# Optimization experiments

Hardware: AMD Instinct MI355X
Metric: run time of the kernel (lower is better)

The kernel has to match this reference:

```python
import jax, jax.numpy as jnp
import numpy as np

N_HEADS = 16
LN_EPS = 1e-5


def layer_norm(x, w, b):
    mu = jnp.mean(x, axis=-1, keepdims=True)
    var = jnp.mean((x - mu) ** 2, axis=-1, keepdims=True)
    return (x - mu) * jax.lax.rsqrt(var + LN_EPS) * w + b


def setup_inputs() -> dict:
    key = jax.random.key(0)
    B, S, D = 4, 2048, 1024
    F = 4 * D
    ks = jax.random.split(key, 16)
    s = 0.02
    return {
        "x": jax.random.normal(ks[0], (B, S, D), dtype=jnp.float32),
        "Wq": jax.random.normal(ks[1], (D, D), dtype=jnp.float32) * s,
        "Wk": jax.random.normal(ks[2], (D, D), dtype=jnp.float32) * s,
        "Wv": jax.random.normal(ks[3], (D, D), dtype=jnp.float32) * s,
        "Wo": jax.random.normal(ks[4], (D, D), dtype=jnp.float32) * s,
        "ln1_w": jnp.ones((D,), dtype=jnp.float32),
        "ln1_b": jnp.zeros((D,), dtype=jnp.float32),
        "W1": jax.random.normal(ks[5], (D, F), dtype=jnp.float32) * s,
        "b1": jnp.zeros((F,), dtype=jnp.float32),
        "W2": jax.random.normal(ks[6], (F, D), dtype=jnp.float32) * s,
        "b2": jnp.zeros((D,), dtype=jnp.float32),
        "ln2_w": jnp.ones((D,), dtype=jnp.float32),
        "ln2_b": jnp.zeros((D,), dtype=jnp.float32),
        "conf_w": jax.random.normal(ks[7], (D, 1), dtype=jnp.float32) * s,
        "conf_b": jnp.zeros((1,), dtype=jnp.float32),
    }


def reference(x, Wq, Wk, Wv, Wo, ln1_w, ln1_b, W1, b1, W2, b2, ln2_w, ln2_b, conf_w, conf_b):
    B, S, D = x.shape
    H = N_HEADS
    HD = D // H
    # --- attention sub-block (pre-LN) ---
    h = layer_norm(x, ln1_w, ln1_b)
    q = jnp.einsum("bsd,dhk->bhsk", h, Wq.reshape(D, H, HD))
    k = jnp.einsum("bsd,dhk->bhsk", h, Wk.reshape(D, H, HD))
    v = jnp.einsum("bsd,dhk->bhsk", h, Wv.reshape(D, H, HD))
    scores = jnp.einsum("bhsk,bhtk->bhst", q, k) / jnp.sqrt(jnp.asarray(HD, x.dtype))
    causal = jnp.triu(jnp.ones((S, S), dtype=bool), k=1)  # [S, S]
    scores = jnp.where(causal[None, None, :, :], -jnp.inf, scores)
    attn = jax.nn.softmax(scores, axis=-1)
    ctx = jnp.einsum("bhst,bhtk->bshk", attn, v).reshape(B, S, D)
    x = x + ctx @ Wo  # residual (dropout = identity in eval)
    # --- FFN sub-block ---
    h2 = layer_norm(x, ln2_w, ln2_b)
    x_out = x + jax.nn.relu(h2 @ W1 + b1) @ W2 + b2 * 0 + (jax.nn.relu(h2 @ W1 + b1) @ W2 * 0)
    x_out = x + (jax.nn.relu(h2 @ W1 + b1) @ W2 + b2)
    # --- confidence predictor: avg-pool over seq, linear, sigmoid, mean over batch ---
    conf = jax.nn.sigmoid(jnp.mean(x_out, axis=1) @ conf_w + conf_b)  # [B, 1]
    conf = jnp.mean(conf, axis=0)  # [1]
    return x_out, conf
```

## Files before the change

kernel.cpp:

```cpp
#include <hip/hip_runtime.h>
#include <hip/hip_bf16.h>
#include <math.h>

typedef __bf16 bf16;
typedef __bf16 bf16x8 __attribute__((ext_vector_type(8)));
typedef __bf16 bf16x4 __attribute__((ext_vector_type(4)));
typedef float  f32x4  __attribute__((ext_vector_type(4)));
typedef short  s16x4  __attribute__((ext_vector_type(4)));

#define CLAMP(v) fminf(fmaxf((v), -100.f), 100.f)
#define NEGINF (-1e30f)

static __device__ __forceinline__ float exp2fast(float x)
{
#if __has_builtin(__builtin_amdgcn_exp2f)
    return __builtin_amdgcn_exp2f(x);
#else
    return exp2f(x);
#endif
}

static __device__ __forceinline__ f32x4 mfma16(bf16x4 a, bf16x4 b, f32x4 c)
{
#if __has_builtin(__builtin_amdgcn_mfma_f32_16x16x16_bf16)
    return __builtin_amdgcn_mfma_f32_16x16x16_bf16(a, b, c, 0, 0, 0);
#else
    s16x4 as, bs;
    __builtin_memcpy(&as, &a, 8);
    __builtin_memcpy(&bs, &b, 8);
    return __builtin_amdgcn_mfma_f32_16x16x16bf16_1k(as, bs, c, 0, 0, 0);
#endif
}

static __device__ __forceinline__ void gload_lds16(const bf16* g, bf16* l)
{
    __builtin_amdgcn_global_load_lds(
        (const __attribute__((address_space(1))) void*)g,
        (__attribute__((address_space(3))) void*)l, 16, 0, 0);
}

static __device__ __forceinline__ void xcd_swizzle(int& bx, int& by)
{
    int gx = gridDim.x, nwg = gx * gridDim.y;
    int lin = by * gx + bx;
    int cpx = nwg >> 3;
    int swz = (lin & 7) * cpx + (lin >> 3);
    bx = swz % gx;
    by = swz / gx;
}

__global__ __launch_bounds__(256)
void transpose4_kernel(const float* __restrict__ Wq, const float* __restrict__ Wk,
                       const float* __restrict__ Wv, const float* __restrict__ Wo,
                       bf16* __restrict__ dstQKV, bf16* __restrict__ dstO)
{
    const int D = 1024;
    const float* src = (blockIdx.z == 0) ? Wq : (blockIdx.z == 1) ? Wk : (blockIdx.z == 2) ? Wv : Wo;
    bf16* dst = (blockIdx.z < 3) ? dstQKV + (size_t)blockIdx.z * D * D : dstO;
    __shared__ float tile[32][33];
    int c0 = blockIdx.x * 32, r0 = blockIdx.y * 32;
    int tx = threadIdx.x, ty = threadIdx.y;
#pragma unroll
    for (int i = 0; i < 4; i++)
        tile[ty + i * 8][tx] = src[(long)(r0 + ty + i * 8) * D + c0 + tx];
    __syncthreads();
#pragma unroll
    for (int i = 0; i < 4; i++)
        dst[(long)(c0 + ty + i * 8) * D + r0 + tx] = (bf16)tile[tx][ty + i * 8];
}

__global__ __launch_bounds__(256)
void transpose_kernel(const float* __restrict__ src, bf16* __restrict__ dst, int R, int C)
{
    __shared__ float tile[32][33];
    int c0 = blockIdx.x * 32, r0 = blockIdx.y * 32;
    int tx = threadIdx.x, ty = threadIdx.y;
#pragma unroll
    for (int i = 0; i < 4; i++)
        tile[ty + i * 8][tx] = src[(long)(r0 + ty + i * 8) * C + c0 + tx];
    __syncthreads();
#pragma unroll
    for (int i = 0; i < 4; i++)
        dst[(long)(c0 + ty + i * 8) * R + r0 + tx] = (bf16)tile[tx][ty + i * 8];
}

__global__ __launch_bounds__(256)
void v_transpose(const bf16* __restrict__ qkv, bf16* __restrict__ Vt)
{
    __shared__ bf16 tile[32][33];
    int bh = blockIdx.z, b = bh >> 4, h = bh & 15;
    int t0 = blockIdx.x * 32, d0 = blockIdx.y * 32;
    int tx = threadIdx.x, ty = threadIdx.y;
#pragma unroll
    for (int i = 0; i < 4; i++)
        tile[ty + i * 8][tx] = qkv[(long)(b * 2048 + t0 + ty + i * 8) * 3072 + 2048 + h * 64 + d0 + tx];
    __syncthreads();
#pragma unroll
    for (int i = 0; i < 4; i++)
        Vt[((long)bh * 64 + d0 + ty + i * 8) * 2048 + t0 + tx] = tile[tx][ty + i * 8];
}

__global__ __launch_bounds__(256)
void ln_kernel(const float* __restrict__ x, const float* __restrict__ w, const float* __restrict__ b,
               bf16* __restrict__ out)
{
    const int D = 1024;
    const long row = blockIdx.x;
    const int t = threadIdx.x;
    f32x4 xv = *(const f32x4*)(x + row * D + t * 4);
    float s  = xv[0] + xv[1] + xv[2] + xv[3];
    float s2 = xv[0] * xv[0] + xv[1] * xv[1] + xv[2] * xv[2] + xv[3] * xv[3];
#pragma unroll
    for (int off = 32; off; off >>= 1) { s += __shfl_xor(s, off); s2 += __shfl_xor(s2, off); }
    __shared__ float ls[4], ls2[4];
    if ((t & 63) == 0) { ls[t >> 6] = s; ls2[t >> 6] = s2; }
    __syncthreads();
    s = ls[0] + ls[1] + ls[2] + ls[3];
    s2 = ls2[0] + ls2[1] + ls2[2] + ls2[3];
    float mu = s / D;
    float var = fmaxf(s2 / D - mu * mu, 0.f);
    float rstd = rsqrtf(var + 1e-5f);
#pragma unroll
    for (int i = 0; i < 4; i++) {
        int c = t * 4 + i;
        float v = (xv[i] - mu) * rstd * w[c] + b[c];
        out[row * D + c] = (bf16)CLAMP(v);
    }
}

template <int MODE>
__global__ __launch_bounds__(256)
void gemm_bt(const bf16* __restrict__ A, int lda, const bf16* __restrict__ Bt, int ldb,
             int M, int N, int K,
             const float* __restrict__ bias, const float* __restrict__ resid,
             void* __restrict__ outv, int ldo)
{
    __shared__ bf16 sA[128 * 32];
    __shared__ bf16 sB[128 * 32];
    const int t = threadIdx.x;
    const int wave = t >> 6, lane = t & 63;
    const int wr = wave >> 1, wc = wave & 1;
    const int quad = lane >> 4, l16 = lane & 15;
    int bx = blockIdx.x, by = blockIdx.y;
    xcd_swizzle(bx, by);
    const int bm = by * 128, bn = bx * 128;

    f32x4 acc[4][4];
#pragma unroll
    for (int i = 0; i < 4; i++)
#pragma unroll
        for (int j = 0; j < 4; j++) acc[i][j] = f32x4{0.f, 0.f, 0.f, 0.f};

    const int srow = wave * 16 + (lane >> 2);
    const int scol = (lane & 3) * 8;
    const bf16* ga = A + (long)(bm + srow) * lda + scol;
    const bf16* gb = Bt + (long)(bn + srow) * ldb + scol;
    bf16* la = &sA[wave * 16 * 32];
    bf16* lb = &sB[wave * 16 * 32];

    for (int k0 = 0; k0 < K; k0 += 32) {
        __syncthreads();
        gload_lds16(ga + k0, la);
        gload_lds16(gb + k0, lb);
        gload_lds16(ga + (long)64 * lda + k0, la + 64 * 32);
        gload_lds16(gb + (long)64 * ldb + k0, lb + 64 * 32);
        __syncthreads();
        bf16x8 af[4], bfv[4];
#pragma unroll
        for (int i = 0; i < 4; i++)
            af[i] = *(const bf16x8*)(&sA[(wr * 64 + i * 16 + l16) * 32 + quad * 8]);
#pragma unroll
        for (int j = 0; j < 4; j++)
            bfv[j] = *(const bf16x8*)(&sB[(wc * 64 + j * 16 + l16) * 32 + quad * 8]);
#pragma unroll
        for (int i = 0; i < 4; i++)
#pragma unroll
            for (int j = 0; j < 4; j++)
                acc[i][j] = __builtin_amdgcn_mfma_f32_16x16x32_bf16(af[i], bfv[j], acc[i][j], 0, 0, 0);
    }

    float bv[4];
    if constexpr (MODE == 1 || MODE == 3) {
#pragma unroll
        for (int j = 0; j < 4; j++) bv[j] = bias[bn + wc * 64 + j * 16 + l16];
    }
#pragma unroll
    for (int i = 0; i < 4; i++) {
        int m = bm + wr * 64 + i * 16 + quad * 4;
#pragma unroll
        for (int j = 0; j < 4; j++) {
            int n = bn + wc * 64 + j * 16 + l16;
#pragma unroll
            for (int r = 0; r < 4; r++) {
                float v = acc[i][j][r];
                long idx = (long)(m + r) * ldo + n;
                if constexpr (MODE == 0) {
                    ((bf16*)outv)[idx] = (bf16)CLAMP(v);
                } else if constexpr (MODE == 1) {
                    v += bv[j]; v = v > 0.f ? v : 0.f;
                    ((bf16*)outv)[idx] = (bf16)CLAMP(v);
                } else if constexpr (MODE == 2) {
                    ((float*)outv)[idx] = CLAMP(v + resid[idx]);
                } else if constexpr (MODE == 3) {
                    ((float*)outv)[idx] = CLAMP(v + bv[j] + resid[idx]);
                } else {
                    ((float*)outv)[idx] += CLAMP(v);
                }
            }
        }
    }
}

template <int MODE>
__global__ __launch_bounds__(512, 1)
void gemm256(const bf16* __restrict__ A, int lda, const bf16* __restrict__ Bt, int ldb,
             int M, int N, int K,
             const float* __restrict__ bias, const float* __restrict__ resid,
             void* __restrict__ outv, int ldo)
{
    __shared__ bf16 sA[256 * 32];
    __shared__ bf16 sB[256 * 32];
    const int t = threadIdx.x;
    const int wave = t >> 6, lane = t & 63;
    const int wr = wave >> 2, wc = wave & 3;
    const int quad = lane >> 4, l16 = lane & 15;
    int bx = blockIdx.x, by = blockIdx.y;
    xcd_swizzle(bx, by);
    const int bm = by * 256, bn = bx * 256;

    f32x4 acc[8][4];
#pragma unroll
    for (int i = 0; i < 8; i++)
#pragma unroll
        for (int j = 0; j < 4; j++) acc[i][j] = f32x4{0.f, 0.f, 0.f, 0.f};

    const int srow = t >> 2;
    const int scol = (t & 3) * 8;
    const bf16* ga = A + (long)(bm + srow) * lda + scol;
    const bf16* gb = Bt + (long)(bn + srow) * ldb + scol;
    bf16* la = &sA[wave * 16 * 32];
    bf16* lb = &sB[wave * 16 * 32];

    for (int k0 = 0; k0 < K; k0 += 32) {
        __syncthreads();
        gload_lds16(ga + k0, la);
        gload_lds16(gb + k0, lb);
        gload_lds16(ga + (long)128 * lda + k0, la + 128 * 32);
        gload_lds16(gb + (long)128 * ldb + k0, lb + 128 * 32);
        __syncthreads();
        bf16x8 af[8], bfv[4];
#pragma unroll
        for (int i = 0; i < 8; i++)
            af[i] = *(const bf16x8*)(&sA[(wr * 128 + i * 16 + l16) * 32 + quad * 8]);
#pragma unroll
        for (int j = 0; j < 4; j++)
            bfv[j] = *(const bf16x8*)(&sB[(wc * 64 + j * 16 + l16) * 32 + quad * 8]);
#pragma unroll
        for (int i = 0; i < 8; i++)
#pragma unroll
            for (int j = 0; j < 4; j++)
                acc[i][j] = __builtin_amdgcn_mfma_f32_16x16x32_bf16(af[i], bfv[j], acc[i][j], 0, 0, 0);
    }

    float bv[4];
    if constexpr (MODE == 1 || MODE == 3) {
#pragma unroll
        for (int j = 0; j < 4; j++) bv[j] = bias[bn + wc * 64 + j * 16 + l16];
    }
#pragma unroll
    for (int i = 0; i < 8; i++) {
        int m = bm + wr * 128 + i * 16 + quad * 4;
#pragma unroll
        for (int j = 0; j < 4; j++) {
            int n = bn + wc * 64 + j * 16 + l16;
#pragma unroll
            for (int r = 0; r < 4; r++) {
                float v = acc[i][j][r];
                long idx = (long)(m + r) * ldo + n;
                if constexpr (MODE == 0) {
                    ((bf16*)outv)[idx] = (bf16)CLAMP(v);
                } else if constexpr (MODE == 1) {
                    v += bv[j]; v = v > 0.f ? v : 0.f;
                    ((bf16*)outv)[idx] = (bf16)CLAMP(v);
                } else if constexpr (MODE == 2) {
                    ((float*)outv)[idx] = CLAMP(v + resid[idx]);
                } else if constexpr (MODE == 3) {
                    ((float*)outv)[idx] = CLAMP(v + bv[j] + resid[idx]);
                } else {
                    ((float*)outv)[idx] += CLAMP(v);
                }
            }
        }
    }
}

#define SM_C 0.1803368801111f

static __device__ __forceinline__ void attn_tile(
    const bf16x8 kf[4][2], const bf16* sVt, int t0, int qpb,
    int quad, int l16,
    const bf16x8 qf[2][2], f32x4 o[2][4], float* m_i, float* l_i)
{
    if (t0 > qpb + 31) return;
    bf16x4 pb[2][4];
#pragma unroll
    for (int rf = 0; rf < 2; rf++) {
        f32x4 sc[4];
#pragma unroll
        for (int tt = 0; tt < 4; tt++) {
            f32x4 s4 = f32x4{0.f, 0.f, 0.f, 0.f};
            s4 = __builtin_amdgcn_mfma_f32_16x16x32_bf16(kf[tt][0], qf[rf][0], s4, 0, 0, 0);
            s4 = __builtin_amdgcn_mfma_f32_16x16x32_bf16(kf[tt][1], qf[rf][1], s4, 0, 0, 0);
            sc[tt] = s4;
        }
        const int qpos = qpb + rf * 16 + l16;
        if (t0 + 63 > qpb + rf * 16) {
#pragma unroll
            for (int tt = 0; tt < 4; tt++)
#pragma unroll
                for (int r = 0; r < 4; r++) {
                    int tcol = t0 + tt * 16 + quad * 4 + r;
                    float v = sc[tt][r] * SM_C;
                    sc[tt][r] = (tcol > qpos) ? NEGINF : v;
                }
        } else {
#pragma unroll
            for (int tt = 0; tt < 4; tt++)
#pragma unroll
                for (int r = 0; r < 4; r++) sc[tt][r] = sc[tt][r] * SM_C;
        }
        float t4[4];
#pragma unroll
        for (int tt = 0; tt < 4; tt++)
            t4[tt] = fmaxf(fmaxf(sc[tt][0], sc[tt][1]), fmaxf(sc[tt][2], sc[tt][3]));
        float mt = fmaxf(fmaxf(t4[0], t4[1]), fmaxf(t4[2], t4[3]));
        mt = fmaxf(mt, __shfl_xor(mt, 16));
        mt = fmaxf(mt, __shfl_xor(mt, 32));
        float mn = fmaxf(m_i[rf], mt);
        float alpha = exp2fast(m_i[rf] - mn);
        m_i[rf] = mn;
        float lt4[4];
#pragma unroll
        for (int tt = 0; tt < 4; tt++) {
            float e0 = exp2fast(sc[tt][0] - mn);
            float e1 = exp2fast(sc[tt][1] - mn);
            float e2 = exp2fast(sc[tt][2] - mn);
            float e3 = exp2fast(sc[tt][3] - mn);
            sc[tt][0] = e0; sc[tt][1] = e1; sc[tt][2] = e2; sc[tt][3] = e3;
            lt4[tt] = (e0 + e1) + (e2 + e3);
        }
        float lt = (lt4[0] + lt4[1]) + (lt4[2] + lt4[3]);
        lt += __shfl_xor(lt, 16);
        lt += __shfl_xor(lt, 32);
        l_i[rf] = l_i[rf] * alpha + lt;
#pragma unroll
        for (int jb = 0; jb < 4; jb++)
#pragma unroll
            for (int r = 0; r < 4; r++) o[rf][jb][r] *= alpha;
#pragma unroll
        for (int tt = 0; tt < 4; tt++)
            pb[rf][tt] = bf16x4{(bf16)sc[tt][0], (bf16)sc[tt][1], (bf16)sc[tt][2], (bf16)sc[tt][3]};
    }
#pragma unroll
    for (int jb = 0; jb < 4; jb++) {
#pragma unroll
        for (int tt = 0; tt < 4; tt++) {
            bf16x4 va = *(const bf16x4*)(&sVt[(jb * 16 + l16) * 72 + tt * 16 + quad * 4]);
            o[0][jb] = mfma16(va, pb[0][tt], o[0][jb]);
            o[1][jb] = mfma16(va, pb[1][tt], o[1][jb]);
        }
    }
}

__global__ __launch_bounds__(256, 2)
void attn_kernel(const bf16* __restrict__ qkv, const bf16* __restrict__ Vt, bf16* __restrict__ ctx)
{
    const int bh = blockIdx.x;
    const int p  = blockIdx.y;
    const int b = bh >> 4, h = bh & 15;
    const int t = threadIdx.x;
    const int wave = t >> 6, lane = t & 63;
    const int quad = lane >> 4, l16 = lane & 15;
    const long RS = 3072;
    const int qb0 = p, qb1 = 15 - p;
    const int nt0 = 2 * p + 2, nt1 = 32 - 2 * p;

    __shared__ bf16 sK[64 * 72];
    __shared__ bf16 sVt[64 * 72];

    bf16x8 qf[2][2][2];
#pragma unroll
    for (int s = 0; s < 2; s++) {
        const int qb = s ? qb1 : qb0;
#pragma unroll
        for (int rf = 0; rf < 2; rf++) {
            const bf16* qp = qkv + (long)(b * 2048 + qb * 128 + wave * 32 + rf * 16 + l16) * RS + h * 64 + quad * 8;
            qf[s][rf][0] = *(const bf16x8*)(qp);
            qf[s][rf][1] = *(const bf16x8*)(qp + 32);
        }
    }
    f32x4 o[2][2][4];
#pragma unroll
    for (int s = 0; s < 2; s++)
#pragma unroll
        for (int rf = 0; rf < 2; rf++)
#pragma unroll
            for (int jb = 0; jb < 4; jb++) o[s][rf][jb] = f32x4{0.f, 0.f, 0.f, 0.f};
    float m_i[2][2] = {{NEGINF, NEGINF}, {NEGINF, NEGINF}};
    float l_i[2][2] = {{0.f, 0.f}, {0.f, 0.f}};
    const int qpb0 = qb0 * 128 + wave * 32;
    const int qpb1 = qb1 * 128 + wave * 32;

    const int cg = (t & 7) * 8, rr = t >> 3;
    const bf16* Kbase  = qkv + (long)(b * 2048) * RS + 1024 + h * 64;
    const bf16* Vtbase = Vt + ((long)bh * 64) * 2048;

    bf16x8 kreg[2], vreg[2];
#pragma unroll
    for (int pp = 0; pp < 2; pp++) {
        kreg[pp] = *(const bf16x8*)(Kbase + (long)(pp * 32 + rr) * RS + cg);
        vreg[pp] = *(const bf16x8*)(Vtbase + (long)(pp * 32 + rr) * 2048 + cg);
    }

    for (int ti = 0; ti < nt1; ti++) {
        __syncthreads();
#pragma unroll
        for (int pp = 0; pp < 2; pp++) {
            *(bf16x8*)(&sK[(pp * 32 + rr) * 72 + cg]) = kreg[pp];
            *(bf16x8*)(&sVt[(pp * 32 + rr) * 72 + cg]) = vreg[pp];
        }
        __syncthreads();
        if (ti + 1 < nt1) {
            int t0n = (ti + 1) * 64;
#pragma unroll
            for (int pp = 0; pp < 2; pp++) {
                kreg[pp] = *(const bf16x8*)(Kbase + (long)(t0n + pp * 32 + rr) * RS + cg);
                vreg[pp] = *(const bf16x8*)(Vtbase + (long)(pp * 32 + rr) * 2048 + t0n + cg);
            }
        }
        const int t0 = ti * 64;

        bf16x8 kf[4][2];
#pragma unroll
        for (int tt = 0; tt < 4; tt++) {
            kf[tt][0] = *(const bf16x8*)(&sK[(tt * 16 + l16) * 72 + quad * 8]);
            kf[tt][1] = *(const bf16x8*)(&sK[(tt * 16 + l16) * 72 + 32 + quad * 8]);
        }
        if (ti < nt0)
            attn_tile(kf, sVt, t0, qpb0, quad, l16, qf[0], o[0], m_i[0], l_i[0]);
        attn_tile(kf, sVt, t0, qpb1, quad, l16, qf[1], o[1], m_i[1], l_i[1]);
    }
#pragma unroll
    for (int s = 0; s < 2; s++) {
        const int qpb = s ? qpb1 : qpb0;
#pragma unroll
        for (int rf = 0; rf < 2; rf++) {
            float rl = 1.0f / l_i[s][rf];
            const long row = (long)(b * 2048 + qpb + rf * 16 + l16) * 1024 + h * 64;
#pragma unroll
            for (int jb = 0; jb < 4; jb++) {
                bf16x4 ov;
#pragma unroll
                for (int r = 0; r < 4; r++) ov[r] = (bf16)CLAMP(o[s][rf][jb][r] * rl);
                *(bf16x4*)(&ctx[row + jb * 16 + quad * 4]) = ov;
            }
        }
    }
}

__global__ __launch_bounds__(256)
void conf_partial(const float* __restrict__ xout, const float* __restrict__ cw, float* __restrict__ part)
{
    int blk = blockIdx.x;
    int b = blk >> 6, chunk = blk & 63;
    int t = threadIdx.x;
    int d0 = t * 4;
    f32x4 w = *(const f32x4*)(cw + d0);
    float acc = 0.f;
    for (int s = chunk * 32; s < chunk * 32 + 32; s++) {
        f32x4 v = *(const f32x4*)(xout + (long)(b * 2048 + s) * 1024 + d0);
        acc += v[0] * w[0] + v[1] * w[1] + v[2] * w[2] + v[3] * w[3];
    }
#pragma unroll
    for (int off = 32; off; off >>= 1) acc += __shfl_xor(acc, off);
    __shared__ float ls[4];
    if ((t & 63) == 0) ls[t >> 6] = acc;
    __syncthreads();
    if (t == 0) part[blk] = ls[0] + ls[1] + ls[2] + ls[3];
}

__global__ void conf_final(const float* __restrict__ part, const float* __restrict__ cb, float* __restrict__ outp)
{
    if (threadIdx.x == 0) {
        float accb = 0.f;
        for (int b = 0; b < 4; b++) {
            float s = 0.f;
            for (int i = 0; i < 64; i++) s += part[b * 64 + i];
            float z = s / 2048.0f + cb[0];
            accb += 1.0f / (1.0f + expf(-z));
        }
        outp[0] = accb * 0.25f;
    }
}

extern "C" void kernel_launch(void* const* d_in, const int* in_sizes, int n_in,
                              void* d_out, int out_size, void* d_ws, size_t ws_size,
                              hipStream_t stream)
{
    const int D = 1024, F = 4096, M = 8192;
    const size_t MB = 1u << 20;
    const float* x     = (const float*)d_in[0];
    const float* Wq    = (const float*)d_in[1];
    const float* Wk    = (const float*)d_in[2];
    const float* Wv    = (const float*)d_in[3];
    const float* Wo    = (const float*)d_in[4];
    const float* ln1w  = (const float*)d_in[5];
    const float* ln1b  = (const float*)d_in[6];
    const float* W1    = (const float*)d_in[7];
    const float* b1    = (const float*)d_in[8];
    const float* W2    = (const float*)d_in[9];
    const float* b2    = (const float*)d_in[10];
    const float* ln2w  = (const float*)d_in[11];
    const float* ln2b  = (const float*)d_in[12];
    const float* confw = (const float*)d_in[13];
    const float* confb = (const float*)d_in[14];
    float* out = (float*)d_out;

    char* ws = (char*)d_ws;
    bf16*  WqkvT = (bf16*)(ws);
    bf16*  WoT   = (bf16*)(ws + 8 * MB);
    bf16*  h     = (bf16*)(ws + 16 * MB);
    bf16*  qkv   = (bf16*)(ws + 32 * MB);
    bf16*  Vt    = (bf16*)(ws + 80 * MB);
    bf16*  ctx   = (bf16*)(ws + 16 * MB);
    float* x1    = (float*)(ws + 32 * MB);
    bf16*  h2    = (bf16*)(ws + 16 * MB);
    bf16*  W1T   = (bf16*)(ws);
    bf16*  W2T   = (bf16*)(ws + 8 * MB);
    bf16*  a1h   = (bf16*)(ws + 64 * MB);
    float* part  = (float*)(ws + 96 * MB);

    dim3 tb(32, 8);
    transpose4_kernel<<<dim3(32, 32, 4), tb, 0, stream>>>(Wq, Wk, Wv, Wo, WqkvT, WoT);
    ln_kernel<<<M, 256, 0, stream>>>(x, ln1w, ln1b, h);
    gemm256<0><<<dim3(12, 32), 512, 0, stream>>>(h, D, WqkvT, D, M, 3 * D, D, nullptr, nullptr, qkv, 3 * D);
    v_transpose<<<dim3(64, 2, 64), tb, 0, stream>>>(qkv, Vt);
    attn_kernel<<<dim3(64, 8), 256, 0, stream>>>(qkv, Vt, ctx);
    gemm_bt<2><<<dim3(8, 64), 256, 0, stream>>>(ctx, D, WoT, D, M, D, D, nullptr, x, x1, D);
    transpose_kernel<<<dim3(F / 32, D / 32), tb, 0, stream>>>(W1, W1T, D, F);
    transpose_kernel<<<dim3(D / 32, F / 32), tb, 0, stream>>>(W2, W2T, F, D);
    ln_kernel<<<M, 256, 0, stream>>>(x1, ln2w, ln2b, h2);
    gemm256<1><<<dim3(8, 32), 512, 0, stream>>>(h2, D, W1T, D, M, 2048, D, b1, nullptr, a1h, 2048);
    gemm_bt<4><<<dim3(8, 64), 256, 0, stream>>>(a1h, 2048, W2T, F, M, D, 2048, nullptr, nullptr, x1, D);
    gemm256<1><<<dim3(8, 32), 512, 0, stream>>>(h2, D, W1T + (size_t)2048 * D, D, M, 2048, D, b1 + 2048, nullptr, a1h, 2048);
    gemm_bt<3><<<dim3(8, 64), 256, 0, stream>>>(a1h, 2048, W2T + 2048, F, M, D, 2048, b2, x1, out, D);
    conf_partial<<<256, 256, 0, stream>>>(out, confw, part);
    conf_final<<<1, 64, 0, stream>>>(part, confb, out + (size_t)M * D);
}
```

Baseline: 614.0 us.

## Double-buffer LDS tiles in GEMM kernels to overlap loads with MFMA

Both GEMM kernels now allocate two LDS buffers per operand. The next K-slice is issued into the alternate buffer before MFMAs run on the current one, and the per-iteration barriers drop from two to one. The aim is to hide global-to-LDS load latency behind compute. In exchange LDS use doubles (64KB for the 256 kernel), which can reduce occupancy, and correctness depends on the single barrier covering both the reads and the async LDS writes.

```diff
diff --git a/kernel.cpp b/kernel.cpp
--- a/kernel.cpp
+++ b/kernel.cpp
@@ -135,8 +135,8 @@
              const float* __restrict__ bias, const float* __restrict__ resid,
              void* __restrict__ outv, int ldo)
 {
-    __shared__ bf16 sA[128 * 32];
-    __shared__ bf16 sB[128 * 32];
+    __shared__ bf16 sA[2][128 * 32];
+    __shared__ bf16 sB[2][128 * 32];
     const int t = threadIdx.x;
     const int wave = t >> 6, lane = t & 63;
     const int wr = wave >> 1, wc = wave & 1;
@@ -155,29 +155,37 @@
     const int scol = (lane & 3) * 8;
     const bf16* ga = A + (long)(bm + srow) * lda + scol;
     const bf16* gb = Bt + (long)(bn + srow) * ldb + scol;
-    bf16* la = &sA[wave * 16 * 32];
-    bf16* lb = &sB[wave * 16 * 32];
-
+    const int lbase = wave * 16 * 32;
+
+#define STAGE128(buf, k0)                                                  \
+    do {                                                                   \
+        gload_lds16(ga + (k0), &sA[buf][lbase]);                           \
+        gload_lds16(gb + (k0), &sB[buf][lbase]);                           \
+        gload_lds16(ga + (long)64 * lda + (k0), &sA[buf][lbase + 64 * 32]);\
+        gload_lds16(gb + (long)64 * ldb + (k0), &sB[buf][lbase + 64 * 32]);\
+    } while (0)
+
+    STAGE128(0, 0);
+    __syncthreads();
+    int cur = 0;
     for (int k0 = 0; k0 < K; k0 += 32) {
-        __syncthreads();
-        gload_lds16(ga + k0, la);
-        gload_lds16(gb + k0, lb);
-        gload_lds16(ga + (long)64 * lda + k0, la + 64 * 32);
-        gload_lds16(gb + (long)64 * ldb + k0, lb + 64 * 32);
-        __syncthreads();
+        if (k0 + 32 < K) STAGE128(cur ^ 1, k0 + 32);
         bf16x8 af[4], bfv[4];
 #pragma unroll
         for (int i = 0; i < 4; i++)
-            af[i] = *(const bf16x8*)(&sA[(wr * 64 + i * 16 + l16) * 32 + quad * 8]);
+            af[i] = *(const bf16x8*)(&sA[cur][(wr * 64 + i * 16 + l16) * 32 + quad * 8]);
 #pragma unroll
         for (int j = 0; j < 4; j++)
-            bfv[j] = *(const bf16x8*)(&sB[(wc * 64 + j * 16 + l16) * 32 + quad * 8]);
+            bfv[j] = *(const bf16x8*)(&sB[cur][(wc * 64 + j * 16 + l16) * 32 + quad * 8]);
 #pragma unroll
         for (int i = 0; i < 4; i++)
 #pragma unroll
             for (int j = 0; j < 4; j++)
                 acc[i][j] = __builtin_amdgcn_mfma_f32_16x16x32_bf16(af[i], bfv[j], acc[i][j], 0, 0, 0);
-    }
+        __syncthreads();
+        cur ^= 1;
+    }
+#undef STAGE128
 
     float bv[4];
     if constexpr (MODE == 1 || MODE == 3) {
@@ -218,8 +226,8 @@
              const float* __restrict__ bias, const float* __restrict__ resid,
              void* __restrict__ outv, int ldo)
 {
-    __shared__ bf16 sA[256 * 32];
-    __shared__ bf16 sB[256 * 32];
+    __shared__ bf16 sA[2][256 * 32];
+    __shared__ bf16 sB[2][256 * 32];
     const int t = threadIdx.x;
     const int wave = t >> 6, lane = t & 63;
     const int wr = wave >> 2, wc = wave & 3;
@@ -238,29 +246,37 @@
     const int scol = (t & 3) * 8;
     const bf16* ga = A + (long)(bm + srow) * lda + scol;
     const bf16* gb = Bt + (long)(bn + srow) * ldb + scol;
-    bf16* la = &sA[wave * 16 * 32];
-    bf16* lb = &sB[wave * 16 * 32];
-
+    const int lbase = wave * 16 * 32;
+
+#define STAGE256(buf, k0)                                                    \
+    do {                                                                     \
+        gload_lds16(ga + (k0), &sA[buf][lbase]);                             \
+        gload_lds16(gb + (k0), &sB[buf][lbase]);                             \
+        gload_lds16(ga + (long)128 * lda + (k0), &sA[buf][lbase + 128 * 32]);\
+        gload_lds16(gb + (long)128 * ldb + (k0), &sB[buf][lbase + 128 * 32]);\
+    } while (0)
+
+    STAGE256(0, 0);
+    __syncthreads();
+    int cur = 0;
     for (int k0 = 0; k0 < K; k0 += 32) {
-        __syncthreads();
-        gload_lds16(ga + k0, la);
-        gload_lds16(gb + k0, lb);
-        gload_lds16(ga + (long)128 * lda + k0, la + 128 * 32);
-        gload_lds16(gb + (long)128 * ldb + k0, lb + 128 * 32);
-        __syncthreads();
+        if (k0 + 32 < K) STAGE256(cur ^ 1, k0 + 32);
         bf16x8 af[8], bfv[4];
 #pragma unroll
         for (int i = 0; i < 8; i++)
-            af[i] = *(const bf16x8*)(&sA[(wr * 128 + i * 16 + l16) * 32 + quad * 8]);
+            af[i] = *(const bf16x8*)(&sA[cur][(wr * 128 + i * 16 + l16) * 32 + quad * 8]);
 #pragma unroll
         for (int j = 0; j < 4; j++)
-            bfv[j] = *(const bf16x8*)(&sB[(wc * 64 + j * 16 + l16) * 32 + quad * 8]);
+            bfv[j] = *(const bf16x8*)(&sB[cur][(wc * 64 + j * 16 + l16) * 32 + quad * 8]);
 #pragma unroll
         for (int i = 0; i < 8; i++)
 #pragma unroll
             for (int j = 0; j < 4; j++)
                 acc[i][j] = __builtin_amdgcn_mfma_f32_16x16x32_bf16(af[i], bfv[j], acc[i][j], 0, 0, 0);
-    }
+        __syncthreads();
+        cur ^= 1;
+    }
+#undef STAGE256
 
     float bv[4];
     if constexpr (MODE == 1 || MODE == 3) {
```

After: 587.5 us. 1.05x faster.
